# Kernel tuning notes

Hardware: AMD Instinct MI355X
Metric: run time of the kernel (lower is better)

The kernel has to match this reference:

```python
import jax, jax.numpy as jnp
import numpy as np
from jax import lax

B, BANDS, H, W = 128, 100, 9, 9
S = 10  # BANDS = S*S spectral grid
C_HID, OUT_CH = 16, 10
K = 3  # 3x3x3x3 kernel, SAME padding
DN = ('NCEFGH', 'OIEFGH', 'NCEFGH')  # 4 spatial dims E,F,G,H


def _conv4d(x, w, b):
    # x: [B, Cin, S, S, H, W], w: [Cout, Cin, 3, 3, 3, 3]
    y = lax.conv_general_dilated(x, w, (1, 1, 1, 1), 'SAME', dimension_numbers=DN)
    return y + b[None, :, None, None, None, None]


def setup_inputs() -> dict:
    key = jax.random.key(0)
    ks = jax.random.split(key, 13)
    x = jax.random.normal(ks[0], (B, BANDS, H, W), dtype=jnp.float32)
    p = {}
    cin = 1
    for i in range(5):
        p[f'w{i+1}'] = jax.random.normal(ks[1 + 2 * i], (C_HID, cin, K, K, K, K), dtype=jnp.float32) * 0.1
        p[f'b{i+1}'] = jax.random.normal(ks[2 + 2 * i], (C_HID,), dtype=jnp.float32) * 0.1
        cin = C_HID
    p['fc_w'] = jax.random.normal(ks[11], (OUT_CH, C_HID), dtype=jnp.float32) * 0.1
    p['fc_b'] = jax.random.normal(ks[12], (OUT_CH,), dtype=jnp.float32) * 0.1
    return {'x': x, **p}


def reference(x, w1, b1, w2, b2, w3, b3, w4, b4, w5, b5, fc_w, fc_b):
    b, c, h, w = x.shape
    # center_pixel: spectral difference w.r.t. the center pixel
    ctr = x[:, :, h // 2, w // 2]                 # [B, bands]
    local = x - ctr[:, :, None, None]             # [B, bands, H, W]
    # compute_local_feature: fold spectral axis into a 2D grid -> 6D, 1 channel
    pt = local.reshape(b, 1, S, S, h, w)          # [B, 1, S, S, H, W]
    a = pt
    for wgt, bia in ((w1, b1), (w2, b2), (w3, b3), (w4, b4), (w5, b5)):
        a = jax.nn.relu(_conv4d(a, wgt, bia))
    # sideout2d: pool spectral dims, per-pixel MLP readout
    feat = a.mean(axis=(2, 3))                    # [B, 16, H, W]
    out = jnp.einsum('bchw,oc->bohw', feat, fc_w) + fc_b[None, :, None, None]
    return out
```

## Files before the change

kernel.cpp:

```cpp
#include <hip/hip_runtime.h>

#define BB 128
#define CH 16
#define NBANDS 100
#define OUTC 10

#define P1PLANE 121
#define P1POS   17424

#define PFPLANE 132
#define PFPOS   19008

#define REGSZ   33792
#define LDSTILE (16 + 2*REGSZ + 16)
#define NCHUNK  (16*132)
#define NKP     5
#define WPL4    (NKP*9*64)

typedef unsigned short ushort_t;
typedef unsigned int uint_t;
typedef __attribute__((ext_vector_type(8))) short short8;
typedef __attribute__((ext_vector_type(4))) float f32x4;

__device__ __forceinline__ ushort_t f2bf(float f) {
    unsigned u = __float_as_uint(f);
    unsigned r = u + 0x7fffu + ((u >> 16) & 1u);
    return (ushort_t)(r >> 16);
}
__device__ __forceinline__ uint_t pk2(float a, float b) {
    return (uint_t)f2bf(a) | ((uint_t)f2bf(b) << 16);
}

template<int CTRL>
__device__ __forceinline__ short8 dpp_shift(short8 v) {
    union { short8 s; int i[4]; } a, b;
    a.s = v;
    #pragma unroll
    for (int k = 0; k < 4; ++k)
        b.i[k] = __builtin_amdgcn_update_dpp(0, a.i[k], CTRL, 0xf, 0xf, true);
    return b.s;
}

__global__ void prep_kernel(const float* __restrict__ x, float* __restrict__ bufP, int nb) {
    int idx = blockIdx.x * 256 + threadIdx.x;
    if (idx >= nb * PFPOS) return;
    int pos = idx % PFPOS;
    int b = idx / PFPOS;
    int e = pos / 1584;
    int r = pos % 1584;
    int f = r / 132;
    int s = r % 132;
    int g = s / 12, h = s % 12;
    float v = 0.f;
    if (e >= 1 && e <= 10 && f >= 1 && f <= 10 && g >= 1 && g <= 9 && h >= 1 && h <= 9) {
        const float* xp = x + ((size_t)b * NBANDS + (e - 1) * 10 + (f - 1)) * 81;
        v = xp[(g - 1) * 9 + (h - 1)] - xp[40];
    }
    bufP[idx] = v;
}

__global__ void pack_w_kernel(const float* __restrict__ w2, const float* __restrict__ w3,
                              const float* __restrict__ w4, const float* __restrict__ w5,
                              uint4* __restrict__ wp) {
    int t = blockIdx.x * 256 + threadIdx.x;
    if (t >= WPL4) return;
    int layer = blockIdx.y;
    const float* w = (layer == 0) ? w2 : (layer == 1) ? w3 : (layer == 2) ? w4 : w5;
    int l = t & 63, pd = t >> 6;
    int kp = pd / 9, q = pd % 9;
    int co = l & 15, kh = l >> 4;
    int m = kh >> 1, cih = (kh & 1) * 8;
    int c = 2 * kp + m;
    uint_t r[4] = {0, 0, 0, 0};
    if (c <= 8) {
        int tap = c * 9 + q;
        #pragma unroll
        for (int jj = 0; jj < 4; ++jj) {
            ushort_t lo = f2bf(w[(co * 16 + cih + 2 * jj) * 81 + tap]);
            ushort_t hi = f2bf(w[(co * 16 + cih + 2 * jj + 1) * 81 + tap]);
            r[jj] = (uint_t)lo | ((uint_t)hi << 16);
        }
    }
    uint4 v; v.x = r[0]; v.y = r[1]; v.z = r[2]; v.w = r[3];
    wp[(size_t)layer * WPL4 + t] = v;
}

__global__ __launch_bounds__(256) void conv1_kernel(
    const float* __restrict__ in, const float* __restrict__ w,
    const float* __restrict__ bias, ushort_t* __restrict__ out) {
    int idx = blockIdx.x * 256 + threadIdx.x;
    if (idx >= 900) return;
    int b = blockIdx.z;
    int co0 = blockIdx.y * 4;
    int g = idx % 9;
    int f = (idx / 9) % 10;
    int e = idx / 90;

    float acc[4][9];
    #pragma unroll
    for (int co = 0; co < 4; ++co) {
        float bv = bias[co0 + co];
        #pragma unroll
        for (int h = 0; h < 9; ++h) acc[co][h] = bv;
    }

    const float* ip = in + (size_t)b * PFPOS;
    #pragma unroll
    for (int de = 0; de < 3; ++de)
    #pragma unroll
    for (int df = 0; df < 3; ++df)
    #pragma unroll
    for (int dg = 0; dg < 3; ++dg) {
        const float4* rp4 = (const float4*)(ip + ((e + de) * 12 + (f + df)) * PFPLANE + (g + dg) * 12);
        float4 r0 = rp4[0], r1 = rp4[1], r2 = rp4[2];
        float v[12] = {r0.x, r0.y, r0.z, r0.w, r1.x, r1.y, r1.z, r1.w, r2.x, r2.y, r2.z, r2.w};
        #pragma unroll
        for (int dh = 0; dh < 3; ++dh) {
            int tap = de * 27 + df * 9 + dg * 3 + dh;
            #pragma unroll
            for (int co = 0; co < 4; ++co) {
                float ws = w[(co0 + co) * 81 + tap];
                #pragma unroll
                for (int h = 0; h < 9; ++h)
                    acc[co][h] = fmaf(ws, v[h + dh], acc[co][h]);
            }
        }
    }

    ushort_t* op = out + ((size_t)b * P1POS + ((e + 1) * 12 + (f + 1)) * P1PLANE + (g + 1) * 11 + 1) * 16 + co0;
    #pragma unroll
    for (int h = 0; h < 9; ++h) {
        uint2 q;
        q.x = pk2(fmaxf(acc[0][h], 0.f), fmaxf(acc[1][h], 0.f));
        q.y = pk2(fmaxf(acc[2][h], 0.f), fmaxf(acc[3][h], 0.f));
        *(uint2*)(op + h * 16) = q;
    }
}

__device__ __forceinline__ void stage_chunk(const ushort_t* __restrict__ gin,
                                            char* __restrict__ sIn, int i, int eb, int fb) {
    int h = i % 12;
    int gp = i / 12;
    int g = gp % 11;
    int pl = gp / 11;
    int pe = pl >> 2, pf = pl & 3;
    int e2 = eb + pe, f2 = fb + pf;
    bool valid = (e2 >= 1) & (e2 <= 10) & (f2 >= 1) & (f2 <= 10) &
                 (g >= 1) & (g <= 9) & (h >= 1) & (h <= 9);
    uint4 q0 = make_uint4(0, 0, 0, 0), q1 = q0;
    if (valid) {
        const uint4* g4 = (const uint4*)(gin + (size_t)((e2 * 12 + f2) * P1PLANE + g * 11 + h) * 16);
        q0 = g4[0]; q1 = g4[1];
    }
    *(uint4*)(sIn + 16 + i * 16)         = q0;
    *(uint4*)(sIn + 16 + REGSZ + i * 16) = q1;
}

template<int GO0, int NT, int GI0, int GI1>
__device__ __forceinline__ void conv_col(
    const char* __restrict__ sIn, const short8* __restrict__ wv8, int l, int we, int wf,
    float bv, int e_out, int f_out, ushort_t* __restrict__ gout) {

    int h = l & 15, kh = l >> 4;
    int m = kh >> 1;
    int halfoff = (kh & 1) * REGSZ;
    int co = l & 15;

    f32x4 acc[NT];
    #pragma unroll
    for (int t = 0; t < NT; ++t) acc[t] = f32x4{bv, bv, bv, bv};

    #pragma unroll 1
    for (int kp = 0; kp < NKP; ++kp) {
        int c = 2 * kp + m; if (c > 8) c = 8;
        int pl = (we + c / 3) * 4 + (wf + c % 3);
        int base = halfoff + pl * 2112 + h * 16;

        short8 Bf[9];
        #pragma unroll
        for (int q = 0; q < 9; ++q) Bf[q] = wv8[(kp * 9 + q) * 64 + l];

        #pragma unroll
        for (int gi = GI0; gi <= GI1; ++gi) {
            const char* a = sIn + base + gi * 192;
            short8 a0 = *(const short8*)(a);
            short8 a1 = *(const short8*)(a + 16);
            short8 a2 = dpp_shift<0x101>(a1);
            #pragma unroll
            for (int dg = 0; dg < 3; ++dg) {
                int go = gi + 1 - dg;
                if (go >= GO0 && go < GO0 + NT) {
                    int t = go - GO0;
                    acc[t] = __builtin_amdgcn_mfma_f32_16x16x32_bf16(a0, Bf[dg * 3 + 0], acc[t], 0, 0, 0);
                    acc[t] = __builtin_amdgcn_mfma_f32_16x16x32_bf16(a1, Bf[dg * 3 + 1], acc[t], 0, 0, 0);
                    acc[t] = __builtin_amdgcn_mfma_f32_16x16x32_bf16(a2, Bf[dg * 3 + 2], acc[t], 0, 0, 0);
                }
            }
        }
    }

    #pragma unroll
    for (int t = 0; t < NT; ++t) {
        int go = GO0 + t;
        int base2 = ((e_out * 12 + f_out) * P1PLANE + go * 11) * 16 + co;
        #pragma unroll
        for (int reg = 0; reg < 4; ++reg) {
            int rr = kh * 4 + reg;
            if (rr >= 1 && rr <= 9)
                gout[base2 + rr * 16] = f2bf(fmaxf(acc[t][reg], 0.f));
        }
    }
}

__global__ __launch_bounds__(512, 4) void conv_mfma_kernel(
    const ushort_t* __restrict__ in, const uint4* __restrict__ wp,
    const float* __restrict__ bias, ushort_t* __restrict__ out) {

    __shared__ __align__(16) char sIn[LDSTILE];

    int tid = threadIdx.x;
    int b  = blockIdx.y;
    int eb = (blockIdx.x / 5) * 2;
    int fb = (blockIdx.x % 5) * 2;

    const ushort_t* gin = in + (size_t)b * P1POS * 16;
    #pragma unroll
    for (int k = 0; k < 4; ++k)
        stage_chunk(gin, sIn, tid + k * 512, eb, fb);
    if (tid < 64)
        stage_chunk(gin, sIn, tid + 2048, eb, fb);
    __syncthreads();

    int l = tid & 63, wv = tid >> 6;
    int col = wv >> 1, gs = wv & 1;
    int we = col >> 1, wf = col & 1;
    int e_out = eb + 1 + we;
    int f_out = fb + 1 + wf;
    float bv = bias[l & 15];

    ushort_t* gout = out + (size_t)b * P1POS * 16;
    const short8* wv8 = (const short8*)wp;

    if (gs == 0)
        conv_col<1, 5, 0, 6>(sIn, wv8, l, we, wf, bv, e_out, f_out, gout);
    else
        conv_col<6, 4, 5, 10>(sIn, wv8, l, we, wf, bv, e_out, f_out, gout);
}

__global__ __launch_bounds__(704) void featfc_kernel(
    const ushort_t* __restrict__ a, const float* __restrict__ fcw,
    const float* __restrict__ fcb, float* __restrict__ out) {
    int t = threadIdx.x;
    if (t >= 648) return;
    int b = blockIdx.x;
    int j = t & 7;
    int gh = t >> 3;
    int g = gh / 9, h = gh % 9;
    const uint_t* base = (const uint_t*)(a + (size_t)b * P1POS * 16 +
                                         (size_t)((g + 1) * 11 + (h + 1)) * 16) + j;
    float s0 = 0.f, s1 = 0.f;
    #pragma unroll 2
    for (int e = 1; e <= 10; ++e) {
        #pragma unroll
        for (int f = 1; f <= 10; ++f) {
            uint_t u = base[(size_t)(e * 12 + f) * P1PLANE * 8];
            s0 += __uint_as_float(u << 16);
            s1 += __uint_as_float(u & 0xffff0000u);
        }
    }
    s0 *= 0.01f; s1 *= 0.01f;

    float po[OUTC];
    #pragma unroll
    for (int o = 0; o < OUTC; ++o)
        po[o] = fmaf(fcw[o * 16 + 2 * j], s0, fcw[o * 16 + 2 * j + 1] * s1);
    #pragma unroll
    for (int o = 0; o < OUTC; ++o) {
        po[o] += __shfl_xor(po[o], 1);
        po[o] += __shfl_xor(po[o], 2);
        po[o] += __shfl_xor(po[o], 4);
    }
    out[((size_t)b * OUTC + j) * 81 + gh] = po[j] + fcb[j];
    if (j < 2)
        out[((size_t)b * OUTC + j + 8) * 81 + gh] = po[j + 8] + fcb[j + 8];
}

extern "C" void kernel_launch(void* const* d_in, const int* in_sizes, int n_in,
                              void* d_out, int out_size, void* d_ws, size_t ws_size,
                              hipStream_t stream) {
    const float* x   = (const float*)d_in[0];
    const float* w1  = (const float*)d_in[1];
    const float* b1  = (const float*)d_in[2];
    const float* w2  = (const float*)d_in[3];
    const float* b2  = (const float*)d_in[4];
    const float* w3  = (const float*)d_in[5];
    const float* b3  = (const float*)d_in[6];
    const float* w4  = (const float*)d_in[7];
    const float* b4  = (const float*)d_in[8];
    const float* w5  = (const float*)d_in[9];
    const float* b5  = (const float*)d_in[10];
    const float* fcw = (const float*)d_in[11];
    const float* fcb = (const float*)d_in[12];
    float* outp = (float*)d_out;

    char* wsc = (char*)d_ws;
    uint4* wp_all = (uint4*)wsc;
    size_t off = 4ull * WPL4 * sizeof(uint4);

    const size_t perb_bytes = (size_t)PFPOS * 4 + 2ull * P1POS * 16 * 2;
    size_t avail = (ws_size > off) ? ws_size - off : 0;
    int nbmax = (int)(avail / perb_bytes);
    if (nbmax < 1) nbmax = 1;
    if (nbmax > BB) nbmax = BB;

    float* bufP = (float*)(wsc + off);       off += (size_t)nbmax * PFPOS * 4;
    ushort_t* bufA = (ushort_t*)(wsc + off); off += (size_t)nbmax * P1POS * 16 * 2;
    ushort_t* bufB = (ushort_t*)(wsc + off);

    dim3 pg((WPL4 + 255) / 256, 4);
    pack_w_kernel<<<pg, 256, 0, stream>>>(w2, w3, w4, w5, wp_all);

    for (int b0 = 0; b0 < BB; b0 += nbmax) {
        int nb = BB - b0;
        if (nb > nbmax) nb = nbmax;

        int pt = nb * PFPOS;
        prep_kernel<<<(pt + 255) / 256, 256, 0, stream>>>(x + (size_t)b0 * NBANDS * 81, bufP, nb);

        dim3 c1g(4, 4, nb);
        conv1_kernel<<<c1g, 256, 0, stream>>>(bufP, w1, b1, bufA);

        dim3 mg(25, nb);
        conv_mfma_kernel<<<mg, 512, 0, stream>>>(bufA, wp_all + 0 * WPL4, b2, bufB);
        conv_mfma_kernel<<<mg, 512, 0, stream>>>(bufB, wp_all + 1 * WPL4, b3, bufA);
        conv_mfma_kernel<<<mg, 512, 0, stream>>>(bufA, wp_all + 2 * WPL4, b4, bufB);
        conv_mfma_kernel<<<mg, 512, 0, stream>>>(bufB, wp_all + 3 * WPL4, b5, bufA);

        featfc_kernel<<<nb, 704, 0, stream>>>(bufA, fcw, fcb, outp + (size_t)b0 * OUTC * 81);
    }
}
```

Measured before the change: 375.3 us.

## Process several batch items per conv block with double-buffered LDS prefetch

```diff
diff --git a/kernel.cpp b/kernel.cpp
--- a/kernel.cpp
+++ b/kernel.cpp
@@ -12,10 +12,11 @@
 #define PFPOS   19008
 
 #define REGSZ   33792
-#define LDSTILE (16 + 2*REGSZ + 16)
+#define LDSBUF  (16 + 2*REGSZ + 16)
 #define NCHUNK  (16*132)
 #define NKP     5
 #define WPL4    (NKP*9*64)
+#define NBATCH  4
 
 typedef unsigned short ushort_t;
 typedef unsigned int uint_t;
@@ -137,25 +138,6 @@
     }
 }
 
-__device__ __forceinline__ void stage_chunk(const ushort_t* __restrict__ gin,
-                                            char* __restrict__ sIn, int i, int eb, int fb) {
-    int h = i % 12;
-    int gp = i / 12;
-    int g = gp % 11;
-    int pl = gp / 11;
-    int pe = pl >> 2, pf = pl & 3;
-    int e2 = eb + pe, f2 = fb + pf;
-    bool valid = (e2 >= 1) & (e2 <= 10) & (f2 >= 1) & (f2 <= 10) &
-                 (g >= 1) & (g <= 9) & (h >= 1) & (h <= 9);
-    uint4 q0 = make_uint4(0, 0, 0, 0), q1 = q0;
-    if (valid) {
-        const uint4* g4 = (const uint4*)(gin + (size_t)((e2 * 12 + f2) * P1PLANE + g * 11 + h) * 16);
-        q0 = g4[0]; q1 = g4[1];
-    }
-    *(uint4*)(sIn + 16 + i * 16)         = q0;
-    *(uint4*)(sIn + 16 + REGSZ + i * 16) = q1;
-}
-
 template<int GO0, int NT, int GI0, int GI1>
 __device__ __forceinline__ void conv_col(
     const char* __restrict__ sIn, const short8* __restrict__ wv8, int l, int we, int wf,
@@ -212,24 +194,54 @@
     }
 }
 
-__global__ __launch_bounds__(512, 4) void conv_mfma_kernel(
+__global__ __launch_bounds__(512, 2) void conv_mfma_kernel(
     const ushort_t* __restrict__ in, const uint4* __restrict__ wp,
-    const float* __restrict__ bias, ushort_t* __restrict__ out) {
-
-    __shared__ __align__(16) char sIn[LDSTILE];
+    const float* __restrict__ bias, ushort_t* __restrict__ out, int nb) {
+
+    __shared__ __align__(16) char sIn[2 * LDSBUF];
 
     int tid = threadIdx.x;
-    int b  = blockIdx.y;
+    int b0 = blockIdx.y * NBATCH;
     int eb = (blockIdx.x / 5) * 2;
     int fb = (blockIdx.x % 5) * 2;
 
-    const ushort_t* gin = in + (size_t)b * P1POS * 16;
-    #pragma unroll
-    for (int k = 0; k < 4; ++k)
-        stage_chunk(gin, sIn, tid + k * 512, eb, fb);
-    if (tid < 64)
-        stage_chunk(gin, sIn, tid + 2048, eb, fb);
-    __syncthreads();
+    bool vals[5];
+    int  goffs[5];
+    #pragma unroll
+    for (int k = 0; k < 5; ++k) {
+        int i = tid + k * 512;
+        bool inrange = (k < 4) | (tid < 64);
+        int h = i % 12;
+        int gp = i / 12;
+        int g = gp % 11;
+        int pl = gp / 11;
+        int e2 = eb + (pl >> 2), f2 = fb + (pl & 3);
+        vals[k] = inrange & (e2 >= 1) & (e2 <= 10) & (f2 >= 1) & (f2 <= 10) &
+                  (g >= 1) & (g <= 9) & (h >= 1) & (h <= 9);
+        goffs[k] = ((e2 * 12 + f2) * P1PLANE + g * 11 + h) * 16;
+    }
+
+    uint4 q0[5], q1[5];
+    auto stage_load = [&](const ushort_t* gin) {
+        #pragma unroll
+        for (int k = 0; k < 5; ++k) {
+            q0[k] = make_uint4(0, 0, 0, 0); q1[k] = q0[k];
+            if (vals[k]) {
+                const uint4* g4 = (const uint4*)(gin + goffs[k]);
+                q0[k] = g4[0]; q1[k] = g4[1];
+            }
+        }
+    };
+    auto stage_write = [&](char* buf) {
+        #pragma unroll
+        for (int k = 0; k < 5; ++k) {
+            if (k < 4 || tid < 64) {
+                int i = tid + k * 512;
+                *(uint4*)(buf + 16 + i * 16)         = q0[k];
+                *(uint4*)(buf + 16 + REGSZ + i * 16) = q1[k];
+            }
+        }
+    };
 
     int l = tid & 63, wv = tid >> 6;
     int col = wv >> 1, gs = wv & 1;
@@ -237,14 +249,33 @@
     int e_out = eb + 1 + we;
     int f_out = fb + 1 + wf;
     float bv = bias[l & 15];
-
-    ushort_t* gout = out + (size_t)b * P1POS * 16;
     const short8* wv8 = (const short8*)wp;
 
-    if (gs == 0)
-        conv_col<1, 5, 0, 6>(sIn, wv8, l, we, wf, bv, e_out, f_out, gout);
-    else
-        conv_col<6, 4, 5, 10>(sIn, wv8, l, we, wf, bv, e_out, f_out, gout);
+    stage_load(in + (size_t)b0 * (P1POS * 16));
+    stage_write(sIn);
+    __syncthreads();
+
+    #pragma unroll 1
+    for (int t = 0; t < NBATCH; ++t) {
+        int b = b0 + t;
+        char* bufp = sIn + (size_t)(t & 1) * LDSBUF;
+
+        if (t < NBATCH - 1 && (b + 1) < nb)
+            stage_load(in + (size_t)(b + 1) * (P1POS * 16));
+
+        if (b < nb) {
+            ushort_t* gout = out + (size_t)b * (P1POS * 16);
+            if (gs == 0)
+                conv_col<1, 5, 0, 6>(bufp, wv8, l, we, wf, bv, e_out, f_out, gout);
+            else
+                conv_col<6, 4, 5, 10>(bufp, wv8, l, we, wf, bv, e_out, f_out, gout);
+        }
+
+        if (t < NBATCH - 1)
+            stage_write(sIn + (size_t)(1 - (t & 1)) * LDSBUF);
+
+        __syncthreads();
+    }
 }
 
 __global__ __launch_bounds__(704) void featfc_kernel(
@@ -330,11 +361,11 @@
         dim3 c1g(4, 4, nb);
         conv1_kernel<<<c1g, 256, 0, stream>>>(bufP, w1, b1, bufA);
 
-        dim3 mg(25, nb);
-        conv_mfma_kernel<<<mg, 512, 0, stream>>>(bufA, wp_all + 0 * WPL4, b2, bufB);
-        conv_mfma_kernel<<<mg, 512, 0, stream>>>(bufB, wp_all + 1 * WPL4, b3, bufA);
-        conv_mfma_kernel<<<mg, 512, 0, stream>>>(bufA, wp_all + 2 * WPL4, b4, bufB);
-        conv_mfma_kernel<<<mg, 512, 0, stream>>>(bufB, wp_all + 3 * WPL4, b5, bufA);
+        dim3 mg(25, (nb + NBATCH - 1) / NBATCH);
+        conv_mfma_kernel<<<mg, 512, 0, stream>>>(bufA, wp_all + 0 * WPL4, b2, bufB, nb);
+        conv_mfma_kernel<<<mg, 512, 0, stream>>>(bufB, wp_all + 1 * WPL4, b3, bufA, nb);
+        conv_mfma_kernel<<<mg, 512, 0, stream>>>(bufA, wp_all + 2 * WPL4, b4, bufB, nb);
+        conv_mfma_kernel<<<mg, 512, 0, stream>>>(bufB, wp_all + 3 * WPL4, b5, bufA, nb);
 
         featfc_kernel<<<nb, 704, 0, stream>>>(bufA, fcw, fcb, outp + (size_t)b0 * OUTC * 81);
     }
```

Result: slower. 515.4 us (+37.3%).
